# Performance work log

Hardware: AMD Instinct MI355X
Metric: run time of the kernel (lower is better)

Reference implementation:

```python
import jax, jax.numpy as jnp
import numpy as np

C_IN = 256   # c_m
C_H = 32     # outer_product_dim
C_Z = 128
B, S, N = 1, 128, 256  # batch, msa depth, n_res
EPS = 1e-5


def setup_inputs() -> dict:
    key = jax.random.key(0)
    ks = jax.random.split(key, 10)
    msa = jax.random.normal(ks[0], (B, S, N, C_IN), dtype=jnp.float32)
    mask = jax.random.uniform(ks[1], (B, S, N), dtype=jnp.float32)
    ln_w = jnp.ones((C_IN,), jnp.float32)
    ln_b = jnp.zeros((C_IN,), jnp.float32)
    # weights stored [in, out] (torch Linear transposed)
    wl = jax.random.normal(ks[2], (C_IN, C_H), jnp.float32) / np.sqrt(C_IN)
    bl = jnp.zeros((C_H,), jnp.float32)
    wr = jax.random.normal(ks[3], (C_IN, C_H), jnp.float32) / np.sqrt(C_IN)
    br = jnp.zeros((C_H,), jnp.float32)
    wo = jax.random.normal(ks[4], (C_H * C_H, C_Z), jnp.float32) / np.sqrt(C_H * C_H)
    bo = jnp.zeros((C_Z,), jnp.float32)
    return {"msa_representation": msa, "msa_mask": mask, "ln_w": ln_w, "ln_b": ln_b,
            "wl": wl, "bl": bl, "wr": wr, "br": br, "wo": wo, "bo": bo}


def _layer_norm(x, w, b):
    mu = jnp.mean(x, axis=-1, keepdims=True)
    var = jnp.var(x, axis=-1, keepdims=True)
    return (x - mu) * jax.lax.rsqrt(var + EPS) * w + b


def reference(msa_representation, msa_mask, ln_w, ln_b, wl, bl, wr, br, wo, bo):
    x = _layer_norm(msa_representation, ln_w, ln_b)            # [b,s,i,c_in]
    A = x @ wl + bl                                            # [b,s,i,c]
    Bm = x @ wr + br                                           # [b,s,j,d]
    m = msa_mask
    A = A * m[..., None]
    Bm = Bm * m[..., None]
    outer = jnp.einsum('bsic,bsjd->bijcd', A, Bm)              # [b,i,j,c,d]
    norm = jnp.clip(jnp.einsum('bsi,bsj->bij', m, m), 1.0, None)
    mean_val = outer / norm[..., None, None]
    b_, i_, j_ = mean_val.shape[:3]
    mean_val = mean_val.reshape(b_, i_, j_, -1)                # [b,i,j,c*d]
    return mean_val @ wo + bo                                  # [b,i,j,c_z]
```

## Files before the change

kernel.cpp:

```cpp
#include <hip/hip_runtime.h>
#include <hip/hip_bf16.h>
#include <stdint.h>

#define SDEP 128
#define NRES 256
#define CZQ 128

typedef __bf16 v8bf __attribute__((ext_vector_type(8)));
typedef __bf16 v4bf __attribute__((ext_vector_type(4)));
typedef float v16f __attribute__((ext_vector_type(16)));
typedef float v4f __attribute__((ext_vector_type(4)));

__device__ __forceinline__ float dpp_wave_sum(float x) {
  float t;
#define STEP(ctrl)                                                         \
  t = __builtin_bit_cast(float, __builtin_amdgcn_update_dpp(               \
          0, __builtin_bit_cast(int, x), ctrl, 0xF, 0xF, true));           \
  x += t;
  STEP(0x111)
  STEP(0x112)
  STEP(0x114)
  STEP(0x118)
  STEP(0x142)
  STEP(0x143)
#undef STEP
  return x;
}
__device__ __forceinline__ float lane63(float x) {
  return __builtin_bit_cast(float,
      __builtin_amdgcn_readlane(__builtin_bit_cast(int, x), 63));
}

__global__ __launch_bounds__(256) void prep_kernel(
    const float* __restrict__ mask, const float* __restrict__ wo,
    const float* __restrict__ wl, const float* __restrict__ wr,
    float* __restrict__ rnorm, __bf16* __restrict__ wot3,
    __bf16* __restrict__ wcat2)
{
  const int b = blockIdx.x, t = threadIdx.x;
  if (b < 256) {
    float acc = 0.f;
    for (int s = 0; s < SDEP; ++s)
      acc += mask[s * NRES + b] * mask[s * NRES + t];
    rnorm[b * NRES + t] = 1.f / fmaxf(acc, 1.f);
  } else if (b < 768) {
    int idx = (b - 256) * 256 + t;
    int q = idx & 31, n = (idx >> 5) & 15, kk = (idx >> 9) & 31, wv = idx >> 14;
    wot3[idx] = (__bf16)wo[(kk * 32 + q) * CZQ + wv * 16 + n];
  } else {
    int idx = (b - 768) * 256 + t;
    int j = idx & 7, n = (idx >> 3) & 31, hf = (idx >> 8) & 1;
    int ks = (idx >> 9) & 15, tile = idx >> 13;
    int k = ks * 16 + hf * 8 + j;
    const float* w = tile ? wr : wl;
    wcat2[idx] = (__bf16)w[k * 32 + n];
  }
}

__global__ __launch_bounds__(256, 1) void projln_kernel(
    const float* __restrict__ msa, const float* __restrict__ lnw,
    const float* __restrict__ lnb, const __bf16* __restrict__ wcat2,
    const float* __restrict__ bl, const float* __restrict__ br,
    const float* __restrict__ mask,
    __bf16* __restrict__ At2, __bf16* __restrict__ Bt2)
{
  __shared__ __bf16 xs[128 * 258];
  __shared__ __bf16 Ls[4 * 64 * 36];
  const int i = blockIdx.x;
  const int w = threadIdx.x >> 6, lane = threadIdx.x & 63;
  const int half = lane >> 5, l31 = lane & 31;

  const float4 wv = ((const float4*)lnw)[lane];
  const float4 bv = ((const float4*)lnb)[lane];

  #pragma unroll 4
  for (int r = 0; r < 32; ++r) {
    const int s = w * 32 + r;
    float4 x = ((const float4*)(msa + ((size_t)s * 256 + i) * 256))[lane];
    float s1 = dpp_wave_sum(x.x + x.y + x.z + x.w);
    float s2 = dpp_wave_sum(x.x * x.x + x.y * x.y + x.z * x.z + x.w * x.w);
    float mu = lane63(s1) * (1.f / 256.f);
    float var = lane63(s2) * (1.f / 256.f) - mu * mu;
    float rs = rsqrtf(var + 1e-5f);
    v4bf o;
    o[0] = (__bf16)((x.x - mu) * rs * wv.x + bv.x);
    o[1] = (__bf16)((x.y - mu) * rs * wv.y + bv.y);
    o[2] = (__bf16)((x.z - mu) * rs * wv.z + bv.z);
    o[3] = (__bf16)((x.w - mu) * rs * wv.w + bv.w);
    *(v4bf*)(xs + s * 258 + lane * 4) = o;
  }

  v16f acc0, acc1;
  #pragma unroll
  for (int r = 0; r < 16; ++r) { acc0[r] = 0.f; acc1[r] = 0.f; }

  const __bf16* xrow = xs + (w * 32 + l31) * 258 + half * 8;
  const __bf16* bbase = wcat2 + half * 256 + l31 * 8;
  #pragma unroll
  for (int ks = 0; ks < 16; ++ks) {
    v8bf a  = *(const v8bf*)(xrow + ks * 16);
    v8bf b0 = *(const v8bf*)(bbase + ks * 512);
    v8bf b1 = *(const v8bf*)(bbase + 8192 + ks * 512);
    acc0 = __builtin_amdgcn_mfma_f32_32x32x16_bf16(a, b0, acc0, 0, 0, 0);
    acc1 = __builtin_amdgcn_mfma_f32_32x32x16_bf16(a, b1, acc1, 0, 0, 0);
  }

  __bf16* Lw = Ls + w * 64 * 36;
  const float bA = bl[l31], bB = br[l31];
  #pragma unroll
  for (int r = 0; r < 16; ++r) {
    int sl = (r & 3) + 8 * (r >> 2) + 4 * half;
    float mv = mask[(w * 32 + sl) * NRES + i];
    Lw[l31 * 36 + sl]        = (__bf16)((acc0[r] + bA) * mv);
    Lw[(32 + l31) * 36 + sl] = (__bf16)((acc1[r] + bB) * mv);
  }

  const int c = lane >> 1, jq = (lane & 1) * 4;
  #pragma unroll
  for (int o = 0; o < 4; ++o) {
    int oct = w * 4 + o;
    v4bf va = *(const v4bf*)(Lw + c * 36 + o * 8 + jq);
    v4bf vb = *(const v4bf*)(Lw + (32 + c) * 36 + o * 8 + jq);
    *(v4bf*)(At2 + ((size_t)i * 16 + oct) * 256 + lane * 4) = va;
    *(v4bf*)(Bt2 + ((size_t)i * 16 + oct) * 256 + lane * 4) = vb;
  }
}

__global__ __launch_bounds__(512, 4) void outer_kernel(
    const __bf16* __restrict__ At2, const __bf16* __restrict__ Bt2,
    const float* __restrict__ rnorm, const __bf16* __restrict__ wot3,
    const float* __restrict__ bo, float* __restrict__ out)
{
  __shared__ __bf16 Ps[32 * 1032];
  const int tid = threadIdx.x;
  const int w = tid >> 6, lane = tid & 63;
  const int half = lane >> 5, l31 = lane & 31;
  const int bx = blockIdx.x;
  const int by = blockIdx.y;
  const int mt = w >> 1;
  const int nh = w & 1;

  const __bf16* Ap = At2 + ((size_t)(by * 4 + mt)) * 4096 + l31 * 8;
  const __bf16* Bp = Bt2 + ((size_t)(bx * 8 + nh * 4)) * 4096 + l31 * 8;

  v16f acc[4];
  #pragma unroll
  for (int t = 0; t < 4; ++t)
    #pragma unroll
    for (int r = 0; r < 16; ++r) acc[t][r] = 0.f;

  #pragma unroll
  for (int ks = 0; ks < 8; ++ks) {
    int off = (ks * 2 + half) * 256;
    v8bf a = *(const v8bf*)(Ap + off);
    #pragma unroll
    for (int t = 0; t < 4; ++t) {
      v8bf b = *(const v8bf*)(Bp + t * 4096 + off);
      acc[t] = __builtin_amdgcn_mfma_f32_32x32x16_bf16(a, b, acc[t], 0, 0, 0);
    }
  }

  #pragma unroll
  for (int t = 0; t < 4; ++t) {
    int jl = nh * 4 + t;
    int p = mt * 8 + jl;
    float rn = rnorm[(by * 4 + mt) * NRES + bx * 8 + jl];
    #pragma unroll
    for (int r = 0; r < 16; ++r) {
      int cc = (r & 3) + 8 * (r >> 2) + 4 * half;
      Ps[p * 1032 + cc * 32 + l31] = (__bf16)(acc[t][r] * rn);
    }
  }
  __syncthreads();

  const int mr = lane & 15, kq = lane >> 4;
  const int z = w * 16 + mr;
  const __bf16* wp = wot3 + (size_t)w * 16384 + mr * 32 + kq * 8;
  const __bf16* p0 = Ps + mr * 1032 + kq * 8;
  v4f acc2[2];
  #pragma unroll
  for (int t = 0; t < 2; ++t)
    #pragma unroll
    for (int r = 0; r < 4; ++r) acc2[t][r] = 0.f;

  #pragma unroll 8
  for (int kk = 0; kk < 32; ++kk) {
    v8bf b  = *(const v8bf*)(wp + kk * 512);
    v8bf a0 = *(const v8bf*)(p0 + kk * 32);
    v8bf a1 = *(const v8bf*)(p0 + 16 * 1032 + kk * 32);
    acc2[0] = __builtin_amdgcn_mfma_f32_16x16x32_bf16(a0, b, acc2[0], 0, 0, 0);
    acc2[1] = __builtin_amdgcn_mfma_f32_16x16x32_bf16(a1, b, acc2[1], 0, 0, 0);
  }

  const float bz = bo[z];
  #pragma unroll
  for (int mt2 = 0; mt2 < 2; ++mt2) {
    #pragma unroll
    for (int r = 0; r < 4; ++r) {
      int p = mt2 * 16 + kq * 4 + r;
      int i = by * 4 + (p >> 3), j = bx * 8 + (p & 7);
      out[((size_t)i * NRES + j) * CZQ + z] = acc2[mt2][r] + bz;
    }
  }
}

extern "C" void kernel_launch(void* const* d_in, const int* in_sizes, int n_in,
                              void* d_out, int out_size, void* d_ws, size_t ws_size,
                              hipStream_t stream) {
  const float* msa  = (const float*)d_in[0];
  const float* mask = (const float*)d_in[1];
  const float* lnw  = (const float*)d_in[2];
  const float* lnb  = (const float*)d_in[3];
  const float* wl   = (const float*)d_in[4];
  const float* bl   = (const float*)d_in[5];
  const float* wr   = (const float*)d_in[6];
  const float* br   = (const float*)d_in[7];
  const float* wo   = (const float*)d_in[8];
  const float* bo   = (const float*)d_in[9];
  float* out = (float*)d_out;

  char* ws = (char*)d_ws;
  __bf16* At2   = (__bf16*)(ws);
  __bf16* Bt2   = (__bf16*)(ws + 2097152);
  float*  rnorm = (float*)(ws + 4194304);
  __bf16* wot3  = (__bf16*)(ws + 4456448);
  __bf16* wcat2 = (__bf16*)(ws + 4718592);

  prep_kernel<<<832, 256, 0, stream>>>(mask, wo, wl, wr, rnorm, wot3, wcat2);
  projln_kernel<<<256, 256, 0, stream>>>(msa, lnw, lnb, wcat2, bl, br, mask,
                                         At2, Bt2);
  outer_kernel<<<dim3(32, 64), 512, 0, stream>>>(At2, Bt2, rnorm, wot3, bo, out);
}
```

Baseline: 159.8 us.

## Fuse prep into projection kernel and enlarge outer-product tiles to 4x16

Merges the preparation kernel (mask norm, weight conversions) into the LayerNorm/projection kernel. Each projection block now converts the wl/wr weights into shared memory itself, and extra blocks compute rnorm and wot3, which removes one launch and one dependency. The outer-product kernel now uses 1024-thread blocks covering 4x16 residue pairs, with each wave computing a 2x2 MFMA tile so A/B fragments are reused. The trade-off is redundant weight conversion per block, doubled shared memory for Ps, and likely lower occupancy in the outer kernel.

Result: slower. 166.1 us (+3.9%).

```diff
diff --git a/kernel.cpp b/kernel.cpp
--- a/kernel.cpp
+++ b/kernel.cpp
@@ -31,49 +31,56 @@
       __builtin_amdgcn_readlane(__builtin_bit_cast(int, x), 63));
 }
 
-__global__ __launch_bounds__(256) void prep_kernel(
-    const float* __restrict__ mask, const float* __restrict__ wo,
-    const float* __restrict__ wl, const float* __restrict__ wr,
-    float* __restrict__ rnorm, __bf16* __restrict__ wot3,
-    __bf16* __restrict__ wcat2)
-{
-  const int b = blockIdx.x, t = threadIdx.x;
-  if (b < 256) {
-    float acc = 0.f;
-    for (int s = 0; s < SDEP; ++s)
-      acc += mask[s * NRES + b] * mask[s * NRES + t];
-    rnorm[b * NRES + t] = 1.f / fmaxf(acc, 1.f);
-  } else if (b < 768) {
-    int idx = (b - 256) * 256 + t;
-    int q = idx & 31, n = (idx >> 5) & 15, kk = (idx >> 9) & 31, wv = idx >> 14;
-    wot3[idx] = (__bf16)wo[(kk * 32 + q) * CZQ + wv * 16 + n];
-  } else {
-    int idx = (b - 768) * 256 + t;
-    int j = idx & 7, n = (idx >> 3) & 31, hf = (idx >> 8) & 1;
-    int ks = (idx >> 9) & 15, tile = idx >> 13;
-    int k = ks * 16 + hf * 8 + j;
-    const float* w = tile ? wr : wl;
-    wcat2[idx] = (__bf16)w[k * 32 + n];
-  }
-}
-
-__global__ __launch_bounds__(256, 1) void projln_kernel(
+__global__ __launch_bounds__(256, 1) void fusedA_kernel(
     const float* __restrict__ msa, const float* __restrict__ lnw,
-    const float* __restrict__ lnb, const __bf16* __restrict__ wcat2,
-    const float* __restrict__ bl, const float* __restrict__ br,
-    const float* __restrict__ mask,
-    __bf16* __restrict__ At2, __bf16* __restrict__ Bt2)
+    const float* __restrict__ lnb, const float* __restrict__ wl,
+    const float* __restrict__ wr, const float* __restrict__ mask,
+    const float* __restrict__ wo, const float* __restrict__ bl,
+    const float* __restrict__ br,
+    __bf16* __restrict__ At2, __bf16* __restrict__ Bt2,
+    float* __restrict__ rnorm, __bf16* __restrict__ wot3)
 {
   __shared__ __bf16 xs[128 * 258];
   __shared__ __bf16 Ls[4 * 64 * 36];
-  const int i = blockIdx.x;
-  const int w = threadIdx.x >> 6, lane = threadIdx.x & 63;
+  __shared__ __bf16 wcs[16384];
+
+  const int bid = blockIdx.x, t = threadIdx.x;
+  if (bid >= 256) {
+    if (bid < 512) {
+      const int b = bid - 256;
+      float acc = 0.f;
+      for (int s = 0; s < SDEP; ++s)
+        acc += mask[s * NRES + b] * mask[s * NRES + t];
+      rnorm[b * NRES + t] = 1.f / fmaxf(acc, 1.f);
+    } else {
+      const int base = (bid - 512) * 4096 + t;
+      #pragma unroll
+      for (int u = 0; u < 16; ++u) {
+        int idx = base + u * 256;
+        int q = idx & 31, n = (idx >> 5) & 15, kk = (idx >> 9) & 31, wv = idx >> 14;
+        wot3[idx] = (__bf16)wo[(kk * 32 + q) * CZQ + wv * 16 + n];
+      }
+    }
+    return;
+  }
+
+  const int i = bid;
+  const int w = t >> 6, lane = t & 63;
   const int half = lane >> 5, l31 = lane & 31;
 
-  const float4 wv = ((const float4*)lnw)[lane];
-  const float4 bv = ((const float4*)lnb)[lane];
-
-  #pragma unroll 4
+  #pragma unroll
+  for (int u = 0; u < 64; ++u) {
+    int idx = u * 256 + t;
+    int j = idx & 7, n = (idx >> 3) & 31, hf = (idx >> 8) & 1;
+    int ks = (idx >> 9) & 15, tile = idx >> 13;
+    const float* wsrc = tile ? wr : wl;
+    wcs[idx] = (__bf16)wsrc[(ks * 16 + hf * 8 + j) * 32 + n];
+  }
+
+  const float4 wv4 = ((const float4*)lnw)[lane];
+  const float4 bv4 = ((const float4*)lnb)[lane];
+
+  #pragma unroll 8
   for (int r = 0; r < 32; ++r) {
     const int s = w * 32 + r;
     float4 x = ((const float4*)(msa + ((size_t)s * 256 + i) * 256))[lane];
@@ -83,19 +90,20 @@
     float var = lane63(s2) * (1.f / 256.f) - mu * mu;
     float rs = rsqrtf(var + 1e-5f);
     v4bf o;
-    o[0] = (__bf16)((x.x - mu) * rs * wv.x + bv.x);
-    o[1] = (__bf16)((x.y - mu) * rs * wv.y + bv.y);
-    o[2] = (__bf16)((x.z - mu) * rs * wv.z + bv.z);
-    o[3] = (__bf16)((x.w - mu) * rs * wv.w + bv.w);
+    o[0] = (__bf16)((x.x - mu) * rs * wv4.x + bv4.x);
+    o[1] = (__bf16)((x.y - mu) * rs * wv4.y + bv4.y);
+    o[2] = (__bf16)((x.z - mu) * rs * wv4.z + bv4.z);
+    o[3] = (__bf16)((x.w - mu) * rs * wv4.w + bv4.w);
     *(v4bf*)(xs + s * 258 + lane * 4) = o;
   }
+  __syncthreads();
 
   v16f acc0, acc1;
   #pragma unroll
   for (int r = 0; r < 16; ++r) { acc0[r] = 0.f; acc1[r] = 0.f; }
 
   const __bf16* xrow = xs + (w * 32 + l31) * 258 + half * 8;
-  const __bf16* bbase = wcat2 + half * 256 + l31 * 8;
+  const __bf16* bbase = wcs + half * 256 + l31 * 8;
   #pragma unroll
   for (int ks = 0; ks < 16; ++ks) {
     v8bf a  = *(const v8bf*)(xrow + ks * 16);
@@ -126,57 +134,66 @@
   }
 }
 
-__global__ __launch_bounds__(512, 4) void outer_kernel(
+__global__ __launch_bounds__(1024, 4) void outer_kernel(
     const __bf16* __restrict__ At2, const __bf16* __restrict__ Bt2,
     const float* __restrict__ rnorm, const __bf16* __restrict__ wot3,
     const float* __restrict__ bo, float* __restrict__ out)
 {
-  __shared__ __bf16 Ps[32 * 1032];
+  __shared__ __bf16 Ps[64 * 1032];
   const int tid = threadIdx.x;
   const int w = tid >> 6, lane = tid & 63;
   const int half = lane >> 5, l31 = lane & 31;
   const int bx = blockIdx.x;
   const int by = blockIdx.y;
-  const int mt = w >> 1;
-  const int nh = w & 1;
-
-  const __bf16* Ap = At2 + ((size_t)(by * 4 + mt)) * 4096 + l31 * 8;
-  const __bf16* Bp = Bt2 + ((size_t)(bx * 8 + nh * 4)) * 4096 + l31 * 8;
-
-  v16f acc[4];
-  #pragma unroll
-  for (int t = 0; t < 4; ++t)
-    #pragma unroll
-    for (int r = 0; r < 16; ++r) acc[t][r] = 0.f;
+  const int mt = w >> 3;
+  const int nt = w & 7;
+
+  const __bf16* Ap = At2 + ((size_t)(by * 4 + mt * 2)) * 4096 + l31 * 8;
+  const __bf16* Bp = Bt2 + ((size_t)(bx * 16 + nt * 2)) * 4096 + l31 * 8;
+
+  v16f acc[2][2];
+  #pragma unroll
+  for (int a = 0; a < 2; ++a)
+    #pragma unroll
+    for (int b = 0; b < 2; ++b)
+      #pragma unroll
+      for (int r = 0; r < 16; ++r) acc[a][b][r] = 0.f;
 
   #pragma unroll
   for (int ks = 0; ks < 8; ++ks) {
     int off = (ks * 2 + half) * 256;
-    v8bf a = *(const v8bf*)(Ap + off);
-    #pragma unroll
-    for (int t = 0; t < 4; ++t) {
-      v8bf b = *(const v8bf*)(Bp + t * 4096 + off);
-      acc[t] = __builtin_amdgcn_mfma_f32_32x32x16_bf16(a, b, acc[t], 0, 0, 0);
+    v8bf a0 = *(const v8bf*)(Ap + off);
+    v8bf a1 = *(const v8bf*)(Ap + 4096 + off);
+    v8bf b0 = *(const v8bf*)(Bp + off);
+    v8bf b1 = *(const v8bf*)(Bp + 4096 + off);
+    acc[0][0] = __builtin_amdgcn_mfma_f32_32x32x16_bf16(a0, b0, acc[0][0], 0, 0, 0);
+    acc[0][1] = __builtin_amdgcn_mfma_f32_32x32x16_bf16(a0, b1, acc[0][1], 0, 0, 0);
+    acc[1][0] = __builtin_amdgcn_mfma_f32_32x32x16_bf16(a1, b0, acc[1][0], 0, 0, 0);
+    acc[1][1] = __builtin_amdgcn_mfma_f32_32x32x16_bf16(a1, b1, acc[1][1], 0, 0, 0);
+  }
+
+  #pragma unroll
+  for (int ti = 0; ti < 2; ++ti) {
+    #pragma unroll
+    for (int tj = 0; tj < 2; ++tj) {
+      int il = mt * 2 + ti, jl = nt * 2 + tj;
+      int p = il * 16 + jl;
+      float rn = rnorm[(by * 4 + il) * NRES + bx * 16 + jl];
+      #pragma unroll
+      for (int r = 0; r < 16; ++r) {
+        int cc = (r & 3) + 8 * (r >> 2) + 4 * half;
+        Ps[p * 1032 + cc * 32 + l31] = (__bf16)(acc[ti][tj][r] * rn);
+      }
     }
   }
-
-  #pragma unroll
-  for (int t = 0; t < 4; ++t) {
-    int jl = nh * 4 + t;
-    int p = mt * 8 + jl;
-    float rn = rnorm[(by * 4 + mt) * NRES + bx * 8 + jl];
-    #pragma unroll
-    for (int r = 0; r < 16; ++r) {
-      int cc = (r & 3) + 8 * (r >> 2) + 4 * half;
-      Ps[p * 1032 + cc * 32 + l31] = (__bf16)(acc[t][r] * rn);
-    }
-  }
   __syncthreads();
 
   const int mr = lane & 15, kq = lane >> 4;
-  const int z = w * 16 + mr;
-  const __bf16* wp = wot3 + (size_t)w * 16384 + mr * 32 + kq * 8;
-  const __bf16* p0 = Ps + mr * 1032 + kq * 8;
+  const int zw = w & 7;
+  const int mbase = (w >> 3) * 2;
+  const int z = zw * 16 + mr;
+  const __bf16* wp = wot3 + (size_t)zw * 16384 + mr * 32 + kq * 8;
+  const __bf16* pA = Ps + (mbase * 16 + mr) * 1032 + kq * 8;
   v4f acc2[2];
   #pragma unroll
   for (int t = 0; t < 2; ++t)
@@ -186,20 +203,20 @@
   #pragma unroll 8
   for (int kk = 0; kk < 32; ++kk) {
     v8bf b  = *(const v8bf*)(wp + kk * 512);
-    v8bf a0 = *(const v8bf*)(p0 + kk * 32);
-    v8bf a1 = *(const v8bf*)(p0 + 16 * 1032 + kk * 32);
+    v8bf a0 = *(const v8bf*)(pA + kk * 32);
+    v8bf a1 = *(const v8bf*)(pA + 16 * 1032 + kk * 32);
     acc2[0] = __builtin_amdgcn_mfma_f32_16x16x32_bf16(a0, b, acc2[0], 0, 0, 0);
     acc2[1] = __builtin_amdgcn_mfma_f32_16x16x32_bf16(a1, b, acc2[1], 0, 0, 0);
   }
 
   const float bz = bo[z];
   #pragma unroll
-  for (int mt2 = 0; mt2 < 2; ++mt2) {
+  for (int t2 = 0; t2 < 2; ++t2) {
     #pragma unroll
     for (int r = 0; r < 4; ++r) {
-      int p = mt2 * 16 + kq * 4 + r;
-      int i = by * 4 + (p >> 3), j = bx * 8 + (p & 7);
-      out[((size_t)i * NRES + j) * CZQ + z] = acc2[mt2][r] + bz;
+      int p = (mbase + t2) * 16 + kq * 4 + r;
+      int i = by * 4 + (p >> 4), j = bx * 16 + (p & 15);
+      out[((size_t)i * NRES + j) * CZQ + z] = acc2[t2][r] + bz;
     }
   }
 }
@@ -224,10 +241,8 @@
   __bf16* Bt2   = (__bf16*)(ws + 2097152);
   float*  rnorm = (float*)(ws + 4194304);
   __bf16* wot3  = (__bf16*)(ws + 4456448);
-  __bf16* wcat2 = (__bf16*)(ws + 4718592);
-
-  prep_kernel<<<832, 256, 0, stream>>>(mask, wo, wl, wr, rnorm, wot3, wcat2);
-  projln_kernel<<<256, 256, 0, stream>>>(msa, lnw, lnb, wcat2, bl, br, mask,
-                                         At2, Bt2);
-  outer_kernel<<<dim3(32, 64), 512, 0, stream>>>(At2, Bt2, rnorm, wot3, bo, out);
-}
+
+  fusedA_kernel<<<544, 256, 0, stream>>>(msa, lnw, lnb, wl, wr, mask, wo,
+                                         bl, br, At2, Bt2, rnorm, wot3);
+  outer_kernel<<<dim3(16, 64), 1024, 0, stream>>>(At2, Bt2, rnorm, wot3, bo, out);
+}
```

## Fuse prep into projection kernel and use split-K 32x32 MFMA for output projection

Applied to the files above, without the earlier changes.

Merges the prep kernel (rnorm, weight repacking) into the LayerNorm/projection kernel, removing one launch. Each block now converts wl/wr to bf16 in shared memory and runs 512 threads, so each wave computes either the left or the right projection. The second GEMM in the outer kernel is rewritten to use 32x32x16 MFMAs with a two-way split over K across waves, reduced through shared memory, in place of the 16x16x32 tiles. This adds redundant per-block weight conversion, extra barriers, and a shared-memory reduction.

New measurement: 155.8 us. -2.5%, faster.

```diff
diff --git a/kernel.cpp b/kernel.cpp
--- a/kernel.cpp
+++ b/kernel.cpp
@@ -9,7 +9,6 @@
 typedef __bf16 v8bf __attribute__((ext_vector_type(8)));
 typedef __bf16 v4bf __attribute__((ext_vector_type(4)));
 typedef float v16f __attribute__((ext_vector_type(16)));
-typedef float v4f __attribute__((ext_vector_type(4)));
 
 __device__ __forceinline__ float dpp_wave_sum(float x) {
   float t;
@@ -31,51 +30,39 @@
       __builtin_amdgcn_readlane(__builtin_bit_cast(int, x), 63));
 }
 
-__global__ __launch_bounds__(256) void prep_kernel(
-    const float* __restrict__ mask, const float* __restrict__ wo,
-    const float* __restrict__ wl, const float* __restrict__ wr,
-    float* __restrict__ rnorm, __bf16* __restrict__ wot3,
-    __bf16* __restrict__ wcat2)
+__global__ __launch_bounds__(512, 2) void fusedA_kernel(
+    const float* __restrict__ msa, const float* __restrict__ lnw,
+    const float* __restrict__ lnb, const float* __restrict__ wl,
+    const float* __restrict__ wr, const float* __restrict__ mask,
+    const float* __restrict__ wo, const float* __restrict__ bl,
+    const float* __restrict__ br,
+    __bf16* __restrict__ At2, __bf16* __restrict__ Bt2,
+    float* __restrict__ rnorm, __bf16* __restrict__ wot4)
 {
-  const int b = blockIdx.x, t = threadIdx.x;
-  if (b < 256) {
-    float acc = 0.f;
-    for (int s = 0; s < SDEP; ++s)
-      acc += mask[s * NRES + b] * mask[s * NRES + t];
-    rnorm[b * NRES + t] = 1.f / fmaxf(acc, 1.f);
-  } else if (b < 768) {
-    int idx = (b - 256) * 256 + t;
-    int q = idx & 31, n = (idx >> 5) & 15, kk = (idx >> 9) & 31, wv = idx >> 14;
-    wot3[idx] = (__bf16)wo[(kk * 32 + q) * CZQ + wv * 16 + n];
-  } else {
-    int idx = (b - 768) * 256 + t;
+  __shared__ __bf16 xs[128 * 258];
+  __shared__ __bf16 wcs[16384];
+  __shared__ __bf16 Ls[8 * 32 * 36];
+
+  const int i = blockIdx.x, t = threadIdx.x;
+  const int w = t >> 6, lane = t & 63;
+  const int half = lane >> 5, l31 = lane & 31;
+  const int sb = w >> 1, nh = w & 1;
+
+  #pragma unroll
+  for (int u = 0; u < 32; ++u) {
+    int idx = u * 512 + t;
     int j = idx & 7, n = (idx >> 3) & 31, hf = (idx >> 8) & 1;
     int ks = (idx >> 9) & 15, tile = idx >> 13;
-    int k = ks * 16 + hf * 8 + j;
-    const float* w = tile ? wr : wl;
-    wcat2[idx] = (__bf16)w[k * 32 + n];
-  }
-}
-
-__global__ __launch_bounds__(256, 1) void projln_kernel(
-    const float* __restrict__ msa, const float* __restrict__ lnw,
-    const float* __restrict__ lnb, const __bf16* __restrict__ wcat2,
-    const float* __restrict__ bl, const float* __restrict__ br,
-    const float* __restrict__ mask,
-    __bf16* __restrict__ At2, __bf16* __restrict__ Bt2)
-{
-  __shared__ __bf16 xs[128 * 258];
-  __shared__ __bf16 Ls[4 * 64 * 36];
-  const int i = blockIdx.x;
-  const int w = threadIdx.x >> 6, lane = threadIdx.x & 63;
-  const int half = lane >> 5, l31 = lane & 31;
-
-  const float4 wv = ((const float4*)lnw)[lane];
-  const float4 bv = ((const float4*)lnb)[lane];
-
-  #pragma unroll 4
-  for (int r = 0; r < 32; ++r) {
-    const int s = w * 32 + r;
+    const float* wsrc = tile ? wr : wl;
+    wcs[idx] = (__bf16)wsrc[(ks * 16 + hf * 8 + j) * 32 + n];
+  }
+
+  const float4 wv4 = ((const float4*)lnw)[lane];
+  const float4 bv4 = ((const float4*)lnb)[lane];
+
+  #pragma unroll 8
+  for (int r = 0; r < 16; ++r) {
+    const int s = sb * 32 + nh * 16 + r;
     float4 x = ((const float4*)(msa + ((size_t)s * 256 + i) * 256))[lane];
     float s1 = dpp_wave_sum(x.x + x.y + x.z + x.w);
     float s2 = dpp_wave_sum(x.x * x.x + x.y * x.y + x.z * x.z + x.w * x.w);
@@ -83,55 +70,72 @@
     float var = lane63(s2) * (1.f / 256.f) - mu * mu;
     float rs = rsqrtf(var + 1e-5f);
     v4bf o;
-    o[0] = (__bf16)((x.x - mu) * rs * wv.x + bv.x);
-    o[1] = (__bf16)((x.y - mu) * rs * wv.y + bv.y);
-    o[2] = (__bf16)((x.z - mu) * rs * wv.z + bv.z);
-    o[3] = (__bf16)((x.w - mu) * rs * wv.w + bv.w);
+    o[0] = (__bf16)((x.x - mu) * rs * wv4.x + bv4.x);
+    o[1] = (__bf16)((x.y - mu) * rs * wv4.y + bv4.y);
+    o[2] = (__bf16)((x.z - mu) * rs * wv4.z + bv4.z);
+    o[3] = (__bf16)((x.w - mu) * rs * wv4.w + bv4.w);
     *(v4bf*)(xs + s * 258 + lane * 4) = o;
   }
-
-  v16f acc0, acc1;
-  #pragma unroll
-  for (int r = 0; r < 16; ++r) { acc0[r] = 0.f; acc1[r] = 0.f; }
-
-  const __bf16* xrow = xs + (w * 32 + l31) * 258 + half * 8;
-  const __bf16* bbase = wcat2 + half * 256 + l31 * 8;
+  __syncthreads();
+
+  v16f acc;
+  #pragma unroll
+  for (int r = 0; r < 16; ++r) acc[r] = 0.f;
+
+  const __bf16* xrow = xs + (sb * 32 + l31) * 258 + half * 8;
+  const __bf16* bbase = wcs + nh * 8192 + half * 256 + l31 * 8;
   #pragma unroll
   for (int ks = 0; ks < 16; ++ks) {
-    v8bf a  = *(const v8bf*)(xrow + ks * 16);
-    v8bf b0 = *(const v8bf*)(bbase + ks * 512);
-    v8bf b1 = *(const v8bf*)(bbase + 8192 + ks * 512);
-    acc0 = __builtin_amdgcn_mfma_f32_32x32x16_bf16(a, b0, acc0, 0, 0, 0);
-    acc1 = __builtin_amdgcn_mfma_f32_32x32x16_bf16(a, b1, acc1, 0, 0, 0);
-  }
-
-  __bf16* Lw = Ls + w * 64 * 36;
-  const float bA = bl[l31], bB = br[l31];
+    v8bf a = *(const v8bf*)(xrow + ks * 16);
+    v8bf b = *(const v8bf*)(bbase + ks * 512);
+    acc = __builtin_amdgcn_mfma_f32_32x32x16_bf16(a, b, acc, 0, 0, 0);
+  }
+
+  __bf16* Lw = Ls + w * 32 * 36;
+  const float bias = (nh ? br : bl)[l31];
   #pragma unroll
   for (int r = 0; r < 16; ++r) {
     int sl = (r & 3) + 8 * (r >> 2) + 4 * half;
-    float mv = mask[(w * 32 + sl) * NRES + i];
-    Lw[l31 * 36 + sl]        = (__bf16)((acc0[r] + bA) * mv);
-    Lw[(32 + l31) * 36 + sl] = (__bf16)((acc1[r] + bB) * mv);
-  }
-
+    float mv = mask[(sb * 32 + sl) * NRES + i];
+    Lw[l31 * 36 + sl] = (__bf16)((acc[r] + bias) * mv);
+  }
+
+  __bf16* dst = nh ? Bt2 : At2;
   const int c = lane >> 1, jq = (lane & 1) * 4;
   #pragma unroll
   for (int o = 0; o < 4; ++o) {
-    int oct = w * 4 + o;
-    v4bf va = *(const v4bf*)(Lw + c * 36 + o * 8 + jq);
-    v4bf vb = *(const v4bf*)(Lw + (32 + c) * 36 + o * 8 + jq);
-    *(v4bf*)(At2 + ((size_t)i * 16 + oct) * 256 + lane * 4) = va;
-    *(v4bf*)(Bt2 + ((size_t)i * 16 + oct) * 256 + lane * 4) = vb;
+    v4bf v = *(const v4bf*)(Lw + c * 36 + o * 8 + jq);
+    *(v4bf*)(dst + ((size_t)i * 16 + sb * 4 + o) * 256 + lane * 4) = v;
+  }
+
+  if (i < 128) {
+    const int b = i * 2 + (t >> 8), col = t & 255;
+    float a0 = 0.f;
+    #pragma unroll 4
+    for (int s = 0; s < SDEP; ++s)
+      a0 += mask[s * NRES + b] * mask[s * NRES + col];
+    rnorm[b * NRES + col] = 1.f / fmaxf(a0, 1.f);
+  } else {
+    #pragma unroll
+    for (int u = 0; u < 2; ++u) {
+      int idx = (i - 128) * 1024 + u * 512 + t;
+      int j = idx & 7, lc = (idx >> 3) & 63, kk = (idx >> 9) & 63, zg = idx >> 15;
+      int k = kk * 16 + (lc >> 5) * 8 + j;
+      int z = zg * 32 + (lc & 31);
+      wot4[idx] = (__bf16)wo[k * CZQ + z];
+    }
   }
 }
 
 __global__ __launch_bounds__(512, 4) void outer_kernel(
     const __bf16* __restrict__ At2, const __bf16* __restrict__ Bt2,
-    const float* __restrict__ rnorm, const __bf16* __restrict__ wot3,
+    const float* __restrict__ rnorm, const __bf16* __restrict__ wot4,
     const float* __restrict__ bo, float* __restrict__ out)
 {
-  __shared__ __bf16 Ps[32 * 1032];
+  __shared__ char smem[66048];
+  __bf16* Ps = (__bf16*)smem;
+  float* red = (float*)smem;
+
   const int tid = threadIdx.x;
   const int w = tid >> 6, lane = tid & 63;
   const int half = lane >> 5, l31 = lane & 31;
@@ -173,33 +177,39 @@
   }
   __syncthreads();
 
-  const int mr = lane & 15, kq = lane >> 4;
-  const int z = w * 16 + mr;
-  const __bf16* wp = wot3 + (size_t)w * 16384 + mr * 32 + kq * 8;
-  const __bf16* p0 = Ps + mr * 1032 + kq * 8;
-  v4f acc2[2];
-  #pragma unroll
-  for (int t = 0; t < 2; ++t)
-    #pragma unroll
-    for (int r = 0; r < 4; ++r) acc2[t][r] = 0.f;
-
-  #pragma unroll 8
+  const int zg = w & 3, kh = w >> 2;
+  const __bf16* wp = wot4 + ((size_t)((zg * 64 + kh * 32) * 64) + half * 32 + l31) * 8;
+  const __bf16* pp = Ps + l31 * 1032 + kh * 512 + half * 8;
+
+  v16f c2;
+  #pragma unroll
+  for (int r = 0; r < 16; ++r) c2[r] = 0.f;
+
+  #pragma unroll 4
   for (int kk = 0; kk < 32; ++kk) {
-    v8bf b  = *(const v8bf*)(wp + kk * 512);
-    v8bf a0 = *(const v8bf*)(p0 + kk * 32);
-    v8bf a1 = *(const v8bf*)(p0 + 16 * 1032 + kk * 32);
-    acc2[0] = __builtin_amdgcn_mfma_f32_16x16x32_bf16(a0, b, acc2[0], 0, 0, 0);
-    acc2[1] = __builtin_amdgcn_mfma_f32_16x16x32_bf16(a1, b, acc2[1], 0, 0, 0);
-  }
-
-  const float bz = bo[z];
-  #pragma unroll
-  for (int mt2 = 0; mt2 < 2; ++mt2) {
-    #pragma unroll
-    for (int r = 0; r < 4; ++r) {
-      int p = mt2 * 16 + kq * 4 + r;
-      int i = by * 4 + (p >> 3), j = bx * 8 + (p & 7);
-      out[((size_t)i * NRES + j) * CZQ + z] = acc2[mt2][r] + bz;
+    v8bf a = *(const v8bf*)(pp + kk * 16);
+    v8bf b = *(const v8bf*)(wp + kk * 512);
+    c2 = __builtin_amdgcn_mfma_f32_32x32x16_bf16(a, b, c2, 0, 0, 0);
+  }
+  __syncthreads();
+
+  if (kh == 1) {
+    #pragma unroll
+    for (int r = 0; r < 16; ++r) {
+      int cc = (r & 3) + 8 * (r >> 2) + 4 * half;
+      red[zg * 1024 + cc * 32 + l31] = c2[r];
+    }
+  }
+  __syncthreads();
+
+  if (kh == 0) {
+    const float bz = bo[zg * 32 + l31];
+    #pragma unroll
+    for (int r = 0; r < 16; ++r) {
+      int cc = (r & 3) + 8 * (r >> 2) + 4 * half;
+      float v = c2[r] + red[zg * 1024 + cc * 32 + l31] + bz;
+      int i = by * 4 + (cc >> 3), j = bx * 8 + (cc & 7);
+      out[((size_t)i * NRES + j) * CZQ + zg * 32 + l31] = v;
     }
   }
 }
@@ -223,11 +233,9 @@
   __bf16* At2   = (__bf16*)(ws);
   __bf16* Bt2   = (__bf16*)(ws + 2097152);
   float*  rnorm = (float*)(ws + 4194304);
-  __bf16* wot3  = (__bf16*)(ws + 4456448);
-  __bf16* wcat2 = (__bf16*)(ws + 4718592);
-
-  prep_kernel<<<832, 256, 0, stream>>>(mask, wo, wl, wr, rnorm, wot3, wcat2);
-  projln_kernel<<<256, 256, 0, stream>>>(msa, lnw, lnb, wcat2, bl, br, mask,
-                                         At2, Bt2);
-  outer_kernel<<<dim3(32, 64), 512, 0, stream>>>(At2, Bt2, rnorm, wot3, bo, out);
-}
+  __bf16* wot4  = (__bf16*)(ws + 4456448);
+
+  fusedA_kernel<<<256, 512, 0, stream>>>(msa, lnw, lnb, wl, wr, mask, wo,
+                                         bl, br, At2, Bt2, rnorm, wot4);
+  outer_kernel<<<dim3(32, 64), 512, 0, stream>>>(At2, Bt2, rnorm, wot4, bo, out);
+}
```
